# Kernel tuning notes

Measured on AMD Instinct MI355X. Metric: run time of the kernel, lower is better.

Reference implementation:

```python
import jax, jax.numpy as jnp
import numpy as np

S, B, C = 7, 2, 20
LAMBDA_COORD, LAMBDA_NOOBJ = 5.0, 0.5
N, T = 16384, 32


def setup_inputs() -> dict:
    key = jax.random.key(0)
    k1, k2, k3 = jax.random.split(key, 3)
    outputs = jax.random.normal(k1, (N, S, S, B * 5 + C), dtype=jnp.float32)
    # center-format normalized boxes [x, y, w, h] in (0, 1)
    target_boxes = jax.random.uniform(k2, (N, T, 4), dtype=jnp.float32)
    target_labels = jax.random.randint(k3, (N, T), 0, C, dtype=jnp.int32)
    return {"outputs": outputs, "target_boxes": target_boxes, "target_labels": target_labels}


def _iou(b1, b2):
    # center-format boxes [..., 4] -> IoU, broadcasting over leading dims
    x11, y11 = b1[..., 0] - b1[..., 2] / 2, b1[..., 1] - b1[..., 3] / 2
    x12, y12 = b1[..., 0] + b1[..., 2] / 2, b1[..., 1] + b1[..., 3] / 2
    x21, y21 = b2[..., 0] - b2[..., 2] / 2, b2[..., 1] - b2[..., 3] / 2
    x22, y22 = b2[..., 0] + b2[..., 2] / 2, b2[..., 1] + b2[..., 3] / 2
    iw = jnp.clip(jnp.minimum(x12, x22) - jnp.maximum(x11, x21), 0.0)
    ih = jnp.clip(jnp.minimum(y12, y22) - jnp.maximum(y11, y21), 0.0)
    inter = iw * ih
    union = b1[..., 2] * b1[..., 3] + b2[..., 2] * b2[..., 3] - inter
    return inter / jnp.maximum(union, 1e-6)


def yolo_v1_loss(outputs, target_boxes, target_labels):
    n = outputs.shape[0]
    pred_boxes = outputs[..., : B * 4].reshape(n, S, S, B, 4)  # [n,S,S,B,4]
    pred_conf = outputs[..., B * 4 : B * 5]                    # [n,S,S,B]
    pred_cls = outputs[..., B * 5 :]                           # [n,S,S,C]

    cell = 1.0 / S
    g = jnp.arange(S, dtype=jnp.float32)
    px = (pred_boxes[..., 0] + g[None, None, :, None]) * cell  # grid_x varies along dim 2
    py = (pred_boxes[..., 1] + g[None, :, None, None]) * cell  # grid_y varies along dim 1
    pred_boxes_g = jnp.stack([px, py, pred_boxes[..., 2], pred_boxes[..., 3]], axis=-1)

    tx, ty, tw, th = (target_boxes[..., i] for i in range(4))
    gxi = jnp.clip((tx / cell).astype(jnp.int32), 0, S - 1)   # [n,T]
    gyi = jnp.clip((ty / cell).astype(jnp.int32), 0, S - 1)
    ox = (tx - gxi.astype(jnp.float32) * cell) / cell
    oy = (ty - gyi.astype(jnp.float32) * cell) / cell

    bidx = jnp.arange(n)[:, None]
    cell_boxes = pred_boxes_g[bidx, gyi, gxi]  # [n,T,B,4]
    cell_conf = pred_conf[bidx, gyi, gxi]      # [n,T,B]
    cell_cls = pred_cls[bidx, gyi, gxi]        # [n,T,C]

    ious = _iou(target_boxes[:, :, None, :], cell_boxes)          # [n,T,B]
    best = jnp.argmax(ious, axis=-1)                              # [n,T]
    best_box = jnp.take_along_axis(cell_boxes, best[..., None, None], axis=2)[:, :, 0]  # [n,T,4]
    best_conf = jnp.take_along_axis(cell_conf, best[..., None], axis=2)[:, :, 0]        # [n,T]

    pw = jnp.maximum(best_box[..., 2], 1e-6)
    ph = jnp.maximum(best_box[..., 3], 1e-6)
    twc = jnp.maximum(tw, 1e-6)
    thc = jnp.maximum(th, 1e-6)
    box_loss = (
        (best_box[..., 0] - ox) ** 2
        + (best_box[..., 1] - oy) ** 2
        + (jnp.sqrt(pw) - jnp.sqrt(twc)) ** 2
        + (jnp.sqrt(ph) - jnp.sqrt(thc)) ** 2
    ).sum(axis=1)                                                # per-image sum over targets

    obj_loss = ((best_conf - 1.0) ** 2).sum(axis=1)

    onehot = jax.nn.one_hot(target_labels, C, dtype=jnp.float32)
    class_loss = jnp.mean((jax.nn.softmax(cell_cls, axis=-1) - onehot) ** 2, axis=-1).sum(axis=1)

    # obj_mask is never set in the original, so noobj covers every cell/box
    noobj_loss = jnp.mean(pred_conf ** 2, axis=(1, 2, 3))

    per_img = LAMBDA_COORD * box_loss + class_loss + obj_loss + LAMBDA_NOOBJ * noobj_loss
    return jnp.mean(per_img)


def reference(outputs, target_boxes, target_labels):
    return yolo_v1_loss(outputs, target_boxes, target_labels)
```

## Files before the change

### kernel.cpp

```cpp
#include <hip/hip_runtime.h>
#include <math.h>

#define TPB 256
constexpr int kS = 7;
constexpr int kB = 2;
constexpr int kC = 20;
constexpr int kT = 32;
constexpr int kCH = kB * 5 + kC;
constexpr int kCells = kS * kS;
constexpr int kImgF = kCells * kCH;

__device__ __forceinline__ float block_reduce(float v, float* red) {
    #pragma unroll
    for (int off = 32; off > 0; off >>= 1)
        v += __shfl_down(v, off, 64);
    const int lane = threadIdx.x & 63;
    const int wave = threadIdx.x >> 6;
    if (lane == 0) red[wave] = v;
    __syncthreads();
    float s = 0.0f;
    if (threadIdx.x == 0) {
        #pragma unroll
        for (int w = 0; w < TPB / 64; w++) s += red[w];
    }
    return s;
}

__global__ __launch_bounds__(TPB) void yolo_stage1(
    const float* __restrict__ outputs,
    const float4* __restrict__ tboxes,
    const int* __restrict__ tlabels,
    float* __restrict__ blocksums,
    int n)
{
    __shared__ float smem[2 * kImgF];
    __shared__ float red[TPB / 64];
    const int tid = threadIdx.x;
    const int img0 = blockIdx.x * 2;
    const int nimg = min(2, n - img0);

    if (nimg == 2) {
        const float4* src = reinterpret_cast<const float4*>(outputs + (size_t)img0 * kImgF);
        float4* dst = reinterpret_cast<float4*>(smem);
        #pragma unroll
        for (int i = 0; i < 3; i++) {
            int idx = tid + i * TPB;
            if (idx < (2 * kImgF) / 4) dst[idx] = src[idx];
        }
    } else {
        const float2* src = reinterpret_cast<const float2*>(outputs + (size_t)img0 * kImgF);
        float2* dst = reinterpret_cast<float2*>(smem);
        for (int idx = tid; idx < kImgF / 2; idx += TPB) dst[idx] = src[idx];
    }
    __syncthreads();

    float local = 0.0f;

    const int nconf = nimg * 2 * kCells;
    if (tid < nconf) {
        const int sub = (tid >= 2 * kCells) ? 1 : 0;
        const int idx = tid - sub * 2 * kCells;
        const float c = smem[sub * kImgF + (idx >> 1) * kCH + 8 + (idx & 1)];
        local += (0.5f / (float)(2 * kCells)) * c * c;
    }

    if (tid < nimg * kT) {
        const int sub = tid >> 5;
        const float4 tb = tboxes[(size_t)img0 * kT + tid];
        const int lab = tlabels[(size_t)img0 * kT + tid];
        const float cellf = 1.0f / 7.0f;
        const float tx = tb.x, ty = tb.y, tw = tb.z, th = tb.w;

        int gxi = (int)(tx / cellf); gxi = min(max(gxi, 0), kS - 1);
        int gyi = (int)(ty / cellf); gyi = min(max(gyi, 0), kS - 1);
        const float ox = (tx - (float)gxi * cellf) / cellf;
        const float oy = (ty - (float)gyi * cellf) / cellf;
        const float* cellp = &smem[sub * kImgF + (gyi * kS + gxi) * kCH];

        const float t_x1 = tx - tw * 0.5f, t_x2 = tx + tw * 0.5f;
        const float t_y1 = ty - th * 0.5f, t_y2 = ty + th * 0.5f;
        const float tarea = tw * th;
        float ious[2], bxs[2], bys[2], bws[2], bhs[2];
        #pragma unroll
        for (int b = 0; b < 2; b++) {
            const float x = cellp[4 * b + 0], y = cellp[4 * b + 1];
            const float w = cellp[4 * b + 2], h = cellp[4 * b + 3];
            const float px = (x + (float)gxi) * cellf;
            const float py = (y + (float)gyi) * cellf;
            const float x21 = px - w * 0.5f, x22 = px + w * 0.5f;
            const float y21 = py - h * 0.5f, y22 = py + h * 0.5f;
            const float iw = fmaxf(fminf(t_x2, x22) - fmaxf(t_x1, x21), 0.0f);
            const float ih = fmaxf(fminf(t_y2, y22) - fmaxf(t_y1, y21), 0.0f);
            const float inter = iw * ih;
            const float uni = tarea + w * h - inter;
            ious[b] = inter / fmaxf(uni, 1e-6f);
            bxs[b] = px; bys[b] = py; bws[b] = w; bhs[b] = h;
        }
        const int best = (ious[1] > ious[0]) ? 1 : 0;

        const float pw = fmaxf(bws[best], 1e-6f), ph = fmaxf(bhs[best], 1e-6f);
        const float twc = fmaxf(tw, 1e-6f), thc = fmaxf(th, 1e-6f);
        const float dx = bxs[best] - ox, dy = bys[best] - oy;
        const float dw = sqrtf(pw) - sqrtf(twc), dh = sqrtf(ph) - sqrtf(thc);
        const float box_loss = dx * dx + dy * dy + dw * dw + dh * dh;

        const float dconf = cellp[8 + best] - 1.0f;
        const float obj_loss = dconf * dconf;

        float m = cellp[10];
        #pragma unroll
        for (int c = 1; c < kC; c++) m = fmaxf(m, cellp[10 + c]);
        float es[kC];
        float ssum = 0.0f;
        #pragma unroll
        for (int c = 0; c < kC; c++) { es[c] = __expf(cellp[10 + c] - m); ssum += es[c]; }
        const float inv = 1.0f / ssum;
        float cl = 0.0f;
        #pragma unroll
        for (int c = 0; c < kC; c++) {
            const float d = es[c] * inv - (c == lab ? 1.0f : 0.0f);
            cl += d * d;
        }

        local += 5.0f * box_loss + obj_loss + cl * (1.0f / (float)kC);
    }

    const float bsum = block_reduce(local, red);
    if (tid == 0) blocksums[blockIdx.x] = bsum;
}

__global__ __launch_bounds__(TPB) void yolo_stage2(
    const float* __restrict__ blocksums, int nblocks, float invn,
    float* __restrict__ out)
{
    __shared__ float red[TPB / 64];
    float local = 0.0f;
    for (int i = threadIdx.x; i < nblocks; i += TPB) local += blocksums[i];
    const float s = block_reduce(local, red);
    if (threadIdx.x == 0) out[0] = s * invn;
}

extern "C" void kernel_launch(void* const* d_in, const int* in_sizes, int n_in,
                              void* d_out, int out_size, void* d_ws, size_t ws_size,
                              hipStream_t stream)
{
    const float* outputs = (const float*)d_in[0];
    const float4* tboxes = (const float4*)d_in[1];
    const int* tlabels = (const int*)d_in[2];
    float* out = (float*)d_out;
    float* blocksums = (float*)d_ws;

    const int n = in_sizes[0] / kImgF;
    const int nblocks = (n + 1) / 2;

    yolo_stage1<<<nblocks, TPB, 0, stream>>>(outputs, tboxes, tlabels, blocksums, n);
    yolo_stage2<<<1, TPB, 0, stream>>>(blocksums, nblocks, 1.0f / (float)n, out);
}
```

Baseline: 159.2 us.

## Fuse reduction stages with atomic last-block finish and four images per block

```diff
diff --git a/kernel.cpp b/kernel.cpp
--- a/kernel.cpp
+++ b/kernel.cpp
@@ -9,6 +9,7 @@
 constexpr int kCH = kB * 5 + kC;
 constexpr int kCells = kS * kS;
 constexpr int kImgF = kCells * kCH;
+constexpr int IMGS = 4;
 
 __device__ __forceinline__ float block_reduce(float v, float* red) {
     #pragma unroll
@@ -26,43 +27,50 @@
     return s;
 }
 
-__global__ __launch_bounds__(TPB) void yolo_stage1(
+__global__ __launch_bounds__(TPB) void yolo_fused(
     const float* __restrict__ outputs,
     const float4* __restrict__ tboxes,
     const int* __restrict__ tlabels,
-    float* __restrict__ blocksums,
-    int n)
+    float* __restrict__ out,
+    float* __restrict__ accum,
+    unsigned* __restrict__ counter,
+    int n, int nblocks, float invn)
 {
-    __shared__ float smem[2 * kImgF];
+    __shared__ float smem[IMGS * kImgF];
     __shared__ float red[TPB / 64];
     const int tid = threadIdx.x;
-    const int img0 = blockIdx.x * 2;
-    const int nimg = min(2, n - img0);
+    const int img0 = blockIdx.x * IMGS;
+    const int nimg = min(IMGS, n - img0);
 
-    if (nimg == 2) {
+    float local = 0.0f;
+    const float kno = 0.5f / (float)(2 * kCells);
+
+    if (nimg == IMGS) {
         const float4* src = reinterpret_cast<const float4*>(outputs + (size_t)img0 * kImgF);
         float4* dst = reinterpret_cast<float4*>(smem);
+        constexpr int NV4 = IMGS * kImgF / 4;
         #pragma unroll
-        for (int i = 0; i < 3; i++) {
-            int idx = tid + i * TPB;
-            if (idx < (2 * kImgF) / 4) dst[idx] = src[idx];
+        for (int i = 0; i < (NV4 + TPB - 1) / TPB; i++) {
+            const int idx = tid + i * TPB;
+            if (idx < NV4) {
+                const float4 v = src[idx];
+                dst[idx] = v;
+                const int base = (4 * idx) % 30;
+                if (base == 8)      local += kno * (v.x * v.x + v.y * v.y);
+                else if (base == 6) local += kno * (v.z * v.z + v.w * v.w);
+            }
         }
     } else {
-        const float2* src = reinterpret_cast<const float2*>(outputs + (size_t)img0 * kImgF);
-        float2* dst = reinterpret_cast<float2*>(smem);
-        for (int idx = tid; idx < kImgF / 2; idx += TPB) dst[idx] = src[idx];
+        const float* srcf = outputs + (size_t)img0 * kImgF;
+        const int tot = nimg * kImgF;
+        for (int i = tid; i < tot; i += TPB) {
+            const float v = srcf[i];
+            smem[i] = v;
+            const int ch = i % kCH;
+            if (ch == 8 || ch == 9) local += kno * v * v;
+        }
     }
     __syncthreads();
-
-    float local = 0.0f;
-
-    const int nconf = nimg * 2 * kCells;
-    if (tid < nconf) {
-        const int sub = (tid >= 2 * kCells) ? 1 : 0;
-        const int idx = tid - sub * 2 * kCells;
-        const float c = smem[sub * kImgF + (idx >> 1) * kCH + 8 + (idx & 1)];
-        local += (0.5f / (float)(2 * kCells)) * c * c;
-    }
 
     if (tid < nimg * kT) {
         const int sub = tid >> 5;
@@ -126,18 +134,17 @@
     }
 
     const float bsum = block_reduce(local, red);
-    if (tid == 0) blocksums[blockIdx.x] = bsum;
-}
 
-__global__ __launch_bounds__(TPB) void yolo_stage2(
-    const float* __restrict__ blocksums, int nblocks, float invn,
-    float* __restrict__ out)
-{
-    __shared__ float red[TPB / 64];
-    float local = 0.0f;
-    for (int i = threadIdx.x; i < nblocks; i += TPB) local += blocksums[i];
-    const float s = block_reduce(local, red);
-    if (threadIdx.x == 0) out[0] = s * invn;
+    if (tid == 0) {
+        atomicAdd(accum, bsum);
+        __threadfence();
+        const unsigned old = atomicAdd(counter, 1u);
+        if (old == (unsigned)(nblocks - 1)) {
+            __threadfence();
+            const float total = atomicAdd(accum, 0.0f);
+            out[0] = total * invn;
+        }
+    }
 }
 
 extern "C" void kernel_launch(void* const* d_in, const int* in_sizes, int n_in,
@@ -148,11 +155,14 @@
     const float4* tboxes = (const float4*)d_in[1];
     const int* tlabels = (const int*)d_in[2];
     float* out = (float*)d_out;
-    float* blocksums = (float*)d_ws;
+    float* accum = (float*)d_ws;
+    unsigned* counter = (unsigned*)((char*)d_ws + 4);
 
     const int n = in_sizes[0] / kImgF;
-    const int nblocks = (n + 1) / 2;
+    const int nblocks = (n + IMGS - 1) / IMGS;
 
-    yolo_stage1<<<nblocks, TPB, 0, stream>>>(outputs, tboxes, tlabels, blocksums, n);
-    yolo_stage2<<<1, TPB, 0, stream>>>(blocksums, nblocks, 1.0f / (float)n, out);
+    hipMemsetAsync(d_ws, 0, 8, stream);
+    yolo_fused<<<nblocks, TPB, 0, stream>>>(outputs, tboxes, tlabels, out,
+                                            accum, counter, n, nblocks,
+                                            1.0f / (float)n);
 }
```

Measured after the change: 245.6 us. 54.2% more time.
